# Performance work log

Hardware: AMD Instinct MI355X
Metric: run time of the kernel (lower is better)

The kernel has to match this reference:

```python
import math
import jax, jax.numpy as jnp
import numpy as np
from jax import lax

# Fixed values for the module's random shift hyperparams (in their legal ranges)
S2, S3, S5, S6 = 2, 1, -1, 1  # p_2_1_0, p_3_1_0, p_5_1_1, p_6_1_0


def setup_inputs() -> dict:
    key = jax.random.key(0)
    k1, k2, k3, k4, k5 = jax.random.split(key, 5)
    n, c, h, w = 16, 112, 48, 48
    x = jax.random.normal(k1, (n, c, h, w), dtype=jnp.float32)
    bound7 = math.sqrt(3.0 / (w * 3))
    p7_w = jax.random.uniform(k2, (3, w), minval=-bound7, maxval=bound7, dtype=jnp.float32)
    p8_w = jax.random.normal(k3, (1, c, h, 1), dtype=jnp.float32) * 0.02
    p19_w = jax.random.normal(k4, (1, c, 1, 1), dtype=jnp.float32) * 0.02
    cb = 1.0 / math.sqrt(c * 3)
    conv_w = jax.random.uniform(k5, (c, c, 1, 3), minval=-cb, maxval=cb, dtype=jnp.float32)
    return {"x": x, "p7_w": p7_w, "p8_w": p8_w, "p19_w": p19_w, "conv_w": conv_w}


def reference(x, p7_w, p8_w, p19_w, conv_w):
    n, c, h, w = x.shape
    hw = h * w
    # t_1: unfold (1,3) dilation (1,3) pad (0,3) -> width shifts of {-3,0,+3}, zero padded
    xp = jnp.pad(x, ((0, 0), (0, 0), (0, 0), (3, 3)))
    t1 = jnp.stack([xp[..., 3 * k: 3 * k + w] for k in range(3)], axis=2)  # (n,c,3,h,w)
    t2 = jnp.roll(x, S2, axis=2)
    t3 = jnp.roll(t1, S3, axis=3)
    t4 = t3.mean(axis=1)                     # (n,3,h,w)
    t5 = jnp.roll(t2, S5, axis=3)
    t6 = jnp.roll(t4, S6, axis=2)
    t7 = jnp.einsum('nkhw,kw->nh', t6, p7_w)  # einsum 'abcd,bdef->aecf' collapsed -> (n,h)
    t8 = p8_w * t5
    t9 = x + t8
    t10 = t8 - t9                             # mathematically -x, kept as written
    # p_11: Conv2d(c,c,(1,3),dilation=(1,2),padding=(0,2)), width-preserving
    t11 = lax.conv_general_dilated(
        t10, conv_w, window_strides=(1, 1), padding=((0, 0), (2, 2)),
        rhs_dilation=(1, 2), dimension_numbers=('NCHW', 'OIHW', 'NCHW'))
    # t_12: unfold (7,1) dilation (2,1) pad (6,0) on t_7 viewed (n,1,h,1)
    t7p = jnp.pad(t7, ((0, 0), (6, 6)))
    t12 = jnp.stack([t7p[:, 2 * k: 2 * k + h] for k in range(7)], axis=1)  # (n,7,h)
    t13 = jnp.maximum(t11, x)
    # t_14 = bmm(x^T, t13)/sqrt(c): (n,hw,hw)
    t14 = jnp.einsum('ncp,ncq->npq', x.reshape(n, c, hw), t13.reshape(n, c, hw)) / math.sqrt(c)
    t15 = jnp.abs(t12)
    t17 = t15.mean(axis=2)                    # (n,7)
    t18 = (t17[:, None, :] - t10.reshape(n, c * h * w // 7, 7)).reshape(n, c, h, w)
    t19 = p19_w * t18
    # t_16 = t7 - t14 (broadcast over last h*w*w of row-block view), t_20 = t7 + t16
    t14r = t14.reshape(n, h, w * h * w)
    t7b = t7[:, :, None]
    t16 = t7b - t14r
    t20 = (t7b + t16).reshape(n, hw, hw)
    t21 = jnp.einsum('ncp,npq->ncq', t19.reshape(n, c, hw), t20) / math.sqrt(hw)
    return t21.reshape(n, c, h, w)
```

## Files before the change

kernel.cpp:

```cpp
#include <hip/hip_runtime.h>

typedef __attribute__((ext_vector_type(8))) short bfrag;
typedef __attribute__((ext_vector_type(4))) float f32x4;

namespace {
constexpr int N_ = 16, C_ = 112, H_ = 48, W_ = 48, HW_ = 2304;
constexpr int NKS = 18;
constexpr int WS_T7 = 0;
constexpr int WS_A = 1024;
constexpr int WS_WPACK = 40960;
constexpr int WS_GBF = 62464;
constexpr int WS_SPART = 177152;
}

__device__ __forceinline__ float f4e(const float4& v, int e) {
  return e == 0 ? v.x : e == 1 ? v.y : e == 2 ? v.z : v.w;
}
__device__ __forceinline__ unsigned short f2bf(float f) {
  unsigned u = __float_as_uint(f);
  return (unsigned short)((u + 0x7FFFu + ((u >> 16) & 1u)) >> 16);
}
__device__ __forceinline__ float bf2f(unsigned short s) {
  return __uint_as_float(((unsigned)s) << 16);
}

__global__ __launch_bounds__(192) void ath_t7(const float* __restrict__ x,
                                              const float* __restrict__ p7,
                                              float* __restrict__ ws) {
  const int h = blockIdx.x, n = blockIdx.y;
  const int tid = threadIdx.x;
  __shared__ float q[48];
  __shared__ float wred[3];
  if (tid < 48) {
    float s = 0.f;
#pragma unroll
    for (int k = 0; k < 3; ++k) {
      int wp = tid + 3 - 3 * k;
      if (wp >= 0 && wp < 48) s += p7[k * 48 + wp];
    }
    q[tid] = s;
  }
  __syncthreads();
  const int c16 = tid / 12, qq = tid - 12 * c16;
  const float qv0 = q[4 * qq], qv1 = q[4 * qq + 1];
  const float qv2 = q[4 * qq + 2], qv3 = q[4 * qq + 3];
  float d = 0.f;
#pragma unroll
  for (int p = 0; p < 7; ++p) {
    const int c = c16 + 16 * p;
    float4 v = *(const float4*)&x[((size_t)n * C_ + c) * HW_ + h * W_ + 4 * qq];
    d += v.x * qv0 + v.y * qv1 + v.z * qv2 + v.w * qv3;
  }
#pragma unroll
  for (int off = 32; off >= 1; off >>= 1) d += __shfl_xor(d, off);
  if ((tid & 63) == 0) wred[tid >> 6] = d;
  __syncthreads();
  if (tid == 0)
    ws[WS_T7 + n * H_ + (h + 2) % 48] =
        (wred[0] + wred[1] + wred[2]) * (1.0f / 112.0f);
}

__global__ __launch_bounds__(256) void ath_gram(const float* __restrict__ x,
                                                const float* __restrict__ cw,
                                                float* __restrict__ ws) {
  const int bid = blockIdx.x;
  const int tid = threadIdx.x;
  if (bid >= 2 * NKS * N_) {
    int idx = (bid - 2 * NKS * N_) * 256 + tid;
    if (idx < 3 * 112 * 32) {
      int kx = idx / (112 * 32);
      int r = idx - kx * 112 * 32;
      int o = r >> 5;
      int i0 = (r & 31) * 4;
      unsigned short v[4];
#pragma unroll
      for (int e = 0; e < 4; ++e) {
        int i = i0 + e;
        v[e] = (i < 112) ? f2bf(cw[o * 336 + i * 3 + kx]) : (unsigned short)0;
      }
      unsigned short* wp = (unsigned short*)(ws + WS_WPACK);
      *(ushort4*)&wp[(kx * 112 + o) * 128 + i0] = make_ushort4(v[0], v[1], v[2], v[3]);
    }
    return;
  }
  const int half = bid & 1;
  const int ks = (bid >> 1) % NKS;
  const int n = bid / (2 * NKS);
  const int k0 = ks * 128;
  const int lane = tid & 63, wv = tid >> 6;
  const int lr = lane & 15, lg = lane >> 4;
  __shared__ __align__(16) unsigned short As[112][136];
  __shared__ __align__(16) unsigned short t7r[136];
  __shared__ float t7s[48];
  __shared__ float s17[8];
  if (tid < 48) t7s[tid] = ws[WS_T7 + n * H_ + tid];
  __syncthreads();
  if (tid < 7) {
    float s = 0.f;
    for (int hh = 0; hh < 48; ++hh) {
      int j = 2 * tid + hh - 6;
      if (j >= 0 && j < 48) s += fabsf(t7s[j]);
    }
    s17[tid] = s * (1.0f / 48.0f);
  }
  if (tid >= 64 && tid < 192) t7r[tid - 64] = f2bf(t7s[(k0 + tid - 64) / 48]);
  if (tid >= 192 && tid < 200) t7r[128 + (tid - 192)] = 0;
  const int ti = wv + 4 * half;
  bfrag breg[4];
  if (ti < 7) {
    const float* bp = &x[((size_t)n * C_ + 16 * ti + lr) * HW_ + k0 + 8 * lg];
#pragma unroll
    for (int kb = 0; kb < 4; ++kb) {
      float4 v0 = *(const float4*)(bp + 32 * kb);
      float4 v1 = *(const float4*)(bp + 32 * kb + 4);
      breg[kb][0] = (short)f2bf(v0.x); breg[kb][1] = (short)f2bf(v0.y);
      breg[kb][2] = (short)f2bf(v0.z); breg[kb][3] = (short)f2bf(v0.w);
      breg[kb][4] = (short)f2bf(v1.x); breg[kb][5] = (short)f2bf(v1.y);
      breg[kb][6] = (short)f2bf(v1.z); breg[kb][7] = (short)f2bf(v1.w);
    }
  }
  __syncthreads();
  const int kq = tid & 31, cg = tid >> 5;
  const int base7 = (k0 + 4 * kq) % 7;
#pragma unroll
  for (int r = 0; r < 14; ++r) {
    const int c = cg + 8 * r;
    float4 v = *(const float4*)&x[((size_t)n * C_ + c) * HW_ + k0 + 4 * kq];
    int cls0 = (base7 + c) % 7;
    unsigned short a4[4];
#pragma unroll
    for (int e = 0; e < 4; ++e) {
      int cl = cls0 + e;
      cl = (cl >= 7) ? cl - 7 : cl;
      a4[e] = f2bf(f4e(v, e) + s17[cl]);
    }
    *(ushort4*)&As[c][4 * kq] = make_ushort4(a4[0], a4[1], a4[2], a4[3]);
  }
  __syncthreads();
  if (ti == 7) {
    const bfrag zero8 = {0, 0, 0, 0, 0, 0, 0, 0};
#pragma unroll
    for (int kb = 0; kb < 4; ++kb)
      breg[kb] = (lr == 0) ? *(const bfrag*)&t7r[8 * lg + 32 * kb] : zero8;
  }
  f32x4 acc[7];
#pragma unroll
  for (int j = 0; j < 7; ++j) acc[j] = (f32x4){0.f, 0.f, 0.f, 0.f};
#pragma unroll
  for (int kb = 0; kb < 4; ++kb) {
#pragma unroll
    for (int tc = 0; tc < 7; ++tc) {
      bfrag a = *(const bfrag*)&As[16 * tc + lr][8 * lg + 32 * kb];
      acc[tc] = __builtin_amdgcn_mfma_f32_16x16x32_bf16(a, breg[kb], acc[tc], 0, 0, 0);
    }
  }
  unsigned short* sp =
      (unsigned short*)(ws + WS_SPART) + (size_t)(n * NKS + ks) * 14336;
#pragma unroll
  for (int tc = 0; tc < 7; ++tc)
#pragma unroll
    for (int e = 0; e < 4; ++e)
      sp[(16 * tc + 4 * lg + e) * 128 + 16 * ti + lr] = f2bf(acc[tc][e]);
}

__global__ __launch_bounds__(128) void ath_assemble(const float* __restrict__ p19,
                                                    float* __restrict__ ws) {
  const int bid = blockIdx.x;
  const int n = bid / 28, g = bid % 28;
  const int tid = threadIdx.x;
  const int cloc = tid >> 5, q = tid & 31;
  const int c = 4 * g + cloc;
  const int i0 = 4 * q;
  const unsigned short* spb = (const unsigned short*)(ws + WS_SPART);
  float s0 = 0.f, s1 = 0.f, s2 = 0.f, s3 = 0.f;
#pragma unroll
  for (int ks = 0; ks < NKS; ++ks) {
    ushort4 t = *(const ushort4*)&spb[(size_t)(n * NKS + ks) * 14336 + c * 128 + i0];
    s0 += bf2f(t.x); s1 += bf2f(t.y); s2 += bf2f(t.z); s3 += bf2f(t.w);
  }
  unsigned short* gb = (unsigned short*)(ws + WS_GBF);
  if (i0 < 112) {
    const float scale = 1.0f / (48.0f * sqrtf(112.0f));
    const float pc = p19[c];
    *(ushort4*)&gb[((size_t)n * C_ + c) * 128 + i0] =
        make_ushort4(f2bf(pc * s0 * scale), f2bf(pc * s1 * scale),
                     f2bf(pc * s2 * scale), f2bf(pc * s3 * scale));
  } else {
    *(ushort4*)&gb[((size_t)n * C_ + c) * 128 + i0] = make_ushort4(0, 0, 0, 0);
    if (i0 == 112) ws[WS_A + n * C_ + c] = p19[c] * s0 * (2.0f / 48.0f);
  }
}

__global__ __launch_bounds__(256) void ath_fused(const float* __restrict__ x,
                                                 const float* __restrict__ ws,
                                                 float* __restrict__ out) {
  const int h = blockIdx.x, n = blockIdx.y;
  const int tid = threadIdx.x;
  const int lane = tid & 63, wv = tid >> 6;
  const int lr = lane & 15, lg = lane >> 4;
  __shared__ __align__(16) unsigned short xT[52][136];
  __shared__ __align__(16) unsigned short buf[112][136];
  __shared__ float sA[112];
  const float* xb = x + (size_t)n * C_ * HW_ + h * W_;
  const unsigned short* wp = (const unsigned short*)(ws + WS_WPACK);
  const unsigned short* gb = (const unsigned short*)(ws + WS_GBF) + (size_t)n * C_ * 128;
  for (int idx = tid; idx < 52 * 24; idx += 256) {
    int r2 = idx / 24, cc = 112 + idx % 24;
    xT[r2][cc] = 0;
  }
  for (int idx = tid; idx < 4 * 112; idx += 256) {
    int rr = idx / 112;
    int r2 = (rr < 2) ? rr : 48 + rr;
    xT[r2][idx % 112] = 0;
  }
  if (tid < 112) sA[tid] = ws[WS_A + n * C_ + tid];
  for (int idx = tid; idx < 672; idx += 256) {
    int i2 = idx / 12, q = idx - i2 * 12;
    float4 a = *(const float4*)&xb[(size_t)(2 * i2) * HW_ + 4 * q];
    float4 b = *(const float4*)&xb[(size_t)(2 * i2 + 1) * HW_ + 4 * q];
#pragma unroll
    for (int e = 0; e < 4; ++e) {
      unsigned pk = (unsigned)f2bf(f4e(a, e)) | ((unsigned)f2bf(f4e(b, e)) << 16);
      *(unsigned*)&xT[4 * q + 2 + e][2 * i2] = pk;
    }
  }
  for (int idx = tid; idx < 1792; idx += 256) {
    int row = idx >> 4, cq = idx & 15;
    *(float4*)&buf[row][cq * 8] = *(const float4*)&wp[(size_t)row * 128 + cq * 8];
  }
  __syncthreads();

  f32x4 acc[6];
#pragma unroll
  for (int j = 0; j < 6; ++j) acc[j] = (f32x4){0.f, 0.f, 0.f, 0.f};
  for (int kx = 0; kx < 3; ++kx) {
    if (kx) {
      __syncthreads();
      for (int idx = tid; idx < 1792; idx += 256) {
        int row = idx >> 4, cq = idx & 15;
        *(float4*)&buf[row][cq * 8] =
            *(const float4*)&wp[(size_t)(kx * 112 + row) * 128 + cq * 8];
      }
      __syncthreads();
    }
#pragma unroll
    for (int j = 0; j < 6; ++j) {
      int t = wv + 4 * j;
      if (t < 21) {
        int m = t / 3, nt = t - 3 * m;
        int o0 = m * 16, w0 = nt * 16;
#pragma unroll
        for (int kb = 0; kb < 4; ++kb) {
          bfrag a = *(const bfrag*)&buf[o0 + lr][8 * lg + 32 * kb];
          bfrag b = *(const bfrag*)&xT[w0 + lr + 2 * kx][8 * lg + 32 * kb];
          acc[j] = __builtin_amdgcn_mfma_f32_16x16x32_bf16(a, b, acc[j], 0, 0, 0);
        }
      }
    }
  }
  unsigned short tv[6][4];
#pragma unroll
  for (int j = 0; j < 6; ++j) {
    int t = wv + 4 * j;
    if (t < 21) {
      int m = t / 3, nt = t - 3 * m;
      int o0 = m * 16, w0 = nt * 16;
#pragma unroll
      for (int e = 0; e < 4; ++e) {
        float xv = bf2f(xT[w0 + lr + 2][o0 + 4 * lg + e]);
        tv[j][e] = f2bf(fmaxf(-acc[j][e], xv));
      }
    }
  }
  __syncthreads();
#pragma unroll
  for (int j = 0; j < 6; ++j) {
    int t = wv + 4 * j;
    if (t < 21) {
      int m = t / 3, nt = t - 3 * m;
      int o0 = m * 16, w0 = nt * 16;
      unsigned pk0 = (unsigned)tv[j][0] | ((unsigned)tv[j][1] << 16);
      unsigned pk1 = (unsigned)tv[j][2] | ((unsigned)tv[j][3] << 16);
      *(unsigned*)&xT[w0 + lr + 2][o0 + 4 * lg] = pk0;
      *(unsigned*)&xT[w0 + lr + 2][o0 + 4 * lg + 2] = pk1;
    }
  }
  for (int idx = tid; idx < 1792; idx += 256) {
    int row = idx >> 4, cq = idx & 15;
    *(float4*)&buf[row][cq * 8] = *(const float4*)&gb[(size_t)row * 128 + cq * 8];
  }
  __syncthreads();

#pragma unroll
  for (int j = 0; j < 6; ++j) {
    int t = wv + 4 * j;
    if (t < 21) {
      int m = t / 3, nt = t - 3 * m;
      int c0 = m * 16, w0 = nt * 16;
      f32x4 acc2 = {0.f, 0.f, 0.f, 0.f};
#pragma unroll
      for (int kb = 0; kb < 4; ++kb) {
        bfrag a = *(const bfrag*)&buf[c0 + lr][8 * lg + 32 * kb];
        bfrag b = *(const bfrag*)&xT[w0 + lr + 2][8 * lg + 32 * kb];
        acc2 = __builtin_amdgcn_mfma_f32_16x16x32_bf16(a, b, acc2, 0, 0, 0);
      }
#pragma unroll
      for (int e = 0; e < 4; ++e) {
        int c = c0 + 4 * lg + e;
        out[((size_t)n * C_ + c) * HW_ + h * W_ + w0 + lr] = sA[c] - acc2[e];
      }
    }
  }
}

extern "C" void kernel_launch(void* const* d_in, const int* in_sizes, int n_in,
                              void* d_out, int out_size, void* d_ws, size_t ws_size,
                              hipStream_t stream) {
  const float* x = (const float*)d_in[0];
  const float* p7 = (const float*)d_in[1];
  const float* p19 = (const float*)d_in[3];
  const float* cw = (const float*)d_in[4];
  float* ws = (float*)d_ws;
  float* out = (float*)d_out;

  ath_t7<<<dim3(H_, N_), 192, 0, stream>>>(x, p7, ws);
  ath_gram<<<2 * NKS * N_ + 42, 256, 0, stream>>>(x, cw, ws);
  ath_assemble<<<N_ * 28, 128, 0, stream>>>(p19, ws);
  ath_fused<<<dim3(H_, N_), 256, 0, stream>>>(x, ws, out);
}
```

Baseline: 45.47 us.

## Fuse four kernels into one cooperative persistent kernel with grid syncs

Replaces the four-kernel launch sequence (t7, gram, assemble, fused conv+bmm) with a single cooperative kernel of 768 blocks that runs each stage in turn, separated by grid.sync. The assemble step (reducing the split-K partials) is folded into the conv stage so it overlaps with loading conv operands. The aim is to remove per-launch overhead and inter-kernel gaps. In exchange it needs cooperative-launch residency (3 blocks/CU, with an occupancy check and fallback to the old path) and pays for grid-wide barriers.

```diff
diff --git a/kernel.cpp b/kernel.cpp
--- a/kernel.cpp
+++ b/kernel.cpp
@@ -1,4 +1,7 @@
 #include <hip/hip_runtime.h>
+#include <hip/hip_cooperative_groups.h>
+
+namespace cg = cooperative_groups;
 
 typedef __attribute__((ext_vector_type(8))) short bfrag;
 typedef __attribute__((ext_vector_type(4))) float f32x4;
@@ -22,6 +25,296 @@
 }
 __device__ __forceinline__ float bf2f(unsigned short s) {
   return __uint_as_float(((unsigned)s) << 16);
+}
+
+__global__ __launch_bounds__(256, 3) void ath_mega(
+    const float* __restrict__ x, const float* __restrict__ p7,
+    const float* __restrict__ p19, const float* __restrict__ cw,
+    float* __restrict__ ws, float* __restrict__ out) {
+  cg::grid_group grid = cg::this_grid();
+  const int bid = blockIdx.x;
+  const int tid = threadIdx.x;
+  const int lane = tid & 63, wv = tid >> 6;
+  const int lr = lane & 15, lg = lane >> 4;
+  __shared__ __align__(16) unsigned char smem[45056];
+
+  {
+    float* q = (float*)smem;
+    float* wred = (float*)(smem + 192);
+    const int h = bid % 48, n = bid / 48;
+    if (tid < 48) {
+      float s = 0.f;
+#pragma unroll
+      for (int k = 0; k < 3; ++k) {
+        int wp = tid + 3 - 3 * k;
+        if (wp >= 0 && wp < 48) s += p7[k * 48 + wp];
+      }
+      q[tid] = s;
+    }
+    __syncthreads();
+    float d = 0.f;
+    if (tid < 192) {
+      const int c16 = tid / 12, qq = tid - 12 * c16;
+      const float qv0 = q[4 * qq], qv1 = q[4 * qq + 1];
+      const float qv2 = q[4 * qq + 2], qv3 = q[4 * qq + 3];
+#pragma unroll
+      for (int p = 0; p < 7; ++p) {
+        const int c = c16 + 16 * p;
+        float4 v = *(const float4*)&x[((size_t)n * C_ + c) * HW_ + h * W_ + 4 * qq];
+        d += v.x * qv0 + v.y * qv1 + v.z * qv2 + v.w * qv3;
+      }
+    }
+#pragma unroll
+    for (int off = 32; off >= 1; off >>= 1) d += __shfl_xor(d, off);
+    if ((tid & 63) == 0 && tid < 192) wred[tid >> 6] = d;
+    __syncthreads();
+    if (tid == 0)
+      ws[WS_T7 + (bid / 48) * H_ + ((bid % 48) + 2) % 48] =
+          (wred[0] + wred[1] + wred[2]) * (1.0f / 112.0f);
+  }
+  grid.sync();
+
+  if (bid < 2 * NKS * N_) {
+    unsigned short(*As)[136] = (unsigned short(*)[136])smem;
+    unsigned short* t7r = (unsigned short*)(smem + 30464);
+    float* t7s = (float*)(smem + 30736);
+    float* s17 = (float*)(smem + 30928);
+    const int half = bid & 1;
+    const int ks = (bid >> 1) % NKS;
+    const int n = bid / (2 * NKS);
+    const int k0 = ks * 128;
+    if (tid < 48) t7s[tid] = ws[WS_T7 + n * H_ + tid];
+    __syncthreads();
+    if (tid < 7) {
+      float s = 0.f;
+      for (int hh = 0; hh < 48; ++hh) {
+        int j = 2 * tid + hh - 6;
+        if (j >= 0 && j < 48) s += fabsf(t7s[j]);
+      }
+      s17[tid] = s * (1.0f / 48.0f);
+    }
+    if (tid >= 64 && tid < 192) t7r[tid - 64] = f2bf(t7s[(k0 + tid - 64) / 48]);
+    if (tid >= 192 && tid < 200) t7r[128 + (tid - 192)] = 0;
+    const int ti = wv + 4 * half;
+    bfrag breg[4];
+    if (ti < 7) {
+      const float* bp = &x[((size_t)n * C_ + 16 * ti + lr) * HW_ + k0 + 8 * lg];
+#pragma unroll
+      for (int kb = 0; kb < 4; ++kb) {
+        float4 v0 = *(const float4*)(bp + 32 * kb);
+        float4 v1 = *(const float4*)(bp + 32 * kb + 4);
+        breg[kb][0] = (short)f2bf(v0.x); breg[kb][1] = (short)f2bf(v0.y);
+        breg[kb][2] = (short)f2bf(v0.z); breg[kb][3] = (short)f2bf(v0.w);
+        breg[kb][4] = (short)f2bf(v1.x); breg[kb][5] = (short)f2bf(v1.y);
+        breg[kb][6] = (short)f2bf(v1.z); breg[kb][7] = (short)f2bf(v1.w);
+      }
+    }
+    __syncthreads();
+    const int kq = tid & 31, cg2 = tid >> 5;
+    const int base7 = (k0 + 4 * kq) % 7;
+#pragma unroll
+    for (int r = 0; r < 14; ++r) {
+      const int c = cg2 + 8 * r;
+      float4 v = *(const float4*)&x[((size_t)n * C_ + c) * HW_ + k0 + 4 * kq];
+      int cls0 = (base7 + c) % 7;
+      unsigned short a4[4];
+#pragma unroll
+      for (int e = 0; e < 4; ++e) {
+        int cl = cls0 + e;
+        cl = (cl >= 7) ? cl - 7 : cl;
+        a4[e] = f2bf(f4e(v, e) + s17[cl]);
+      }
+      *(ushort4*)&As[c][4 * kq] = make_ushort4(a4[0], a4[1], a4[2], a4[3]);
+    }
+    __syncthreads();
+    if (ti == 7) {
+      const bfrag zero8 = {0, 0, 0, 0, 0, 0, 0, 0};
+#pragma unroll
+      for (int kb = 0; kb < 4; ++kb)
+        breg[kb] = (lr == 0) ? *(const bfrag*)&t7r[8 * lg + 32 * kb] : zero8;
+    }
+    f32x4 acc[7];
+#pragma unroll
+    for (int j = 0; j < 7; ++j) acc[j] = (f32x4){0.f, 0.f, 0.f, 0.f};
+#pragma unroll
+    for (int kb = 0; kb < 4; ++kb) {
+#pragma unroll
+      for (int tc = 0; tc < 7; ++tc) {
+        bfrag a = *(const bfrag*)&As[16 * tc + lr][8 * lg + 32 * kb];
+        acc[tc] = __builtin_amdgcn_mfma_f32_16x16x32_bf16(a, breg[kb], acc[tc], 0, 0, 0);
+      }
+    }
+    unsigned short* sp =
+        (unsigned short*)(ws + WS_SPART) + (size_t)(n * NKS + ks) * 14336;
+#pragma unroll
+    for (int tc = 0; tc < 7; ++tc)
+#pragma unroll
+      for (int e = 0; e < 4; ++e)
+        sp[(16 * tc + 4 * lg + e) * 128 + 16 * ti + lr] = f2bf(acc[tc][e]);
+  } else if (bid < 2 * NKS * N_ + 42) {
+    int idx = (bid - 2 * NKS * N_) * 256 + tid;
+    if (idx < 3 * 112 * 32) {
+      int kx = idx / (112 * 32);
+      int r = idx - kx * 112 * 32;
+      int o = r >> 5;
+      int i0 = (r & 31) * 4;
+      unsigned short v[4];
+#pragma unroll
+      for (int e = 0; e < 4; ++e) {
+        int i = i0 + e;
+        v[e] = (i < 112) ? f2bf(cw[o * 336 + i * 3 + kx]) : (unsigned short)0;
+      }
+      unsigned short* wp = (unsigned short*)(ws + WS_WPACK);
+      *(ushort4*)&wp[(kx * 112 + o) * 128 + i0] = make_ushort4(v[0], v[1], v[2], v[3]);
+    }
+  }
+  grid.sync();
+
+  const int h = bid % 48, n = bid / 48;
+  unsigned short(*xT)[136] = (unsigned short(*)[136])smem;
+  unsigned short(*buf)[136] = (unsigned short(*)[136])(smem + 14144);
+  float* sA = (float*)(smem + 44608);
+  const float* xb = x + (size_t)n * C_ * HW_ + h * W_;
+  const unsigned short* wp = (const unsigned short*)(ws + WS_WPACK);
+  const unsigned short* gb =
+      (const unsigned short*)(ws + WS_GBF) + (size_t)n * C_ * 128;
+  {
+    for (int idx = tid; idx < 52 * 24; idx += 256) {
+      int r2 = idx / 24, cc = 112 + idx % 24;
+      xT[r2][cc] = 0;
+    }
+    for (int idx = tid; idx < 4 * 112; idx += 256) {
+      int rr = idx / 112;
+      int r2 = (rr < 2) ? rr : 48 + rr;
+      xT[r2][idx % 112] = 0;
+    }
+    for (int idx = tid; idx < 672; idx += 256) {
+      int i2 = idx / 12, q = idx - i2 * 12;
+      float4 a = *(const float4*)&xb[(size_t)(2 * i2) * HW_ + 4 * q];
+      float4 b = *(const float4*)&xb[(size_t)(2 * i2 + 1) * HW_ + 4 * q];
+#pragma unroll
+      for (int e = 0; e < 4; ++e) {
+        unsigned pk = (unsigned)f2bf(f4e(a, e)) | ((unsigned)f2bf(f4e(b, e)) << 16);
+        *(unsigned*)&xT[4 * q + 2 + e][2 * i2] = pk;
+      }
+    }
+    for (int idx = tid; idx < 1792; idx += 256) {
+      int row = idx >> 4, cq = idx & 15;
+      *(float4*)&buf[row][cq * 8] = *(const float4*)&wp[(size_t)row * 128 + cq * 8];
+    }
+    if (tid < 75) {
+      int L = bid * 75 + tid;
+      if (L < N_ * C_ * 32) {
+        int n2 = L / 3584;
+        int r = L - n2 * 3584;
+        int c2 = r >> 5;
+        int i0 = 4 * (r & 31);
+        const unsigned short* spb = (const unsigned short*)(ws + WS_SPART);
+        float s0 = 0.f, s1 = 0.f, s2 = 0.f, s3 = 0.f;
+#pragma unroll
+        for (int ks2 = 0; ks2 < NKS; ++ks2) {
+          ushort4 t =
+              *(const ushort4*)&spb[(size_t)(n2 * NKS + ks2) * 14336 + c2 * 128 + i0];
+          s0 += bf2f(t.x); s1 += bf2f(t.y); s2 += bf2f(t.z); s3 += bf2f(t.w);
+        }
+        unsigned short* gbw = (unsigned short*)(ws + WS_GBF);
+        if (i0 < 112) {
+          const float scale = 1.0f / (48.0f * sqrtf(112.0f));
+          const float pc = p19[c2];
+          *(ushort4*)&gbw[((size_t)n2 * C_ + c2) * 128 + i0] =
+              make_ushort4(f2bf(pc * s0 * scale), f2bf(pc * s1 * scale),
+                           f2bf(pc * s2 * scale), f2bf(pc * s3 * scale));
+        } else {
+          *(ushort4*)&gbw[((size_t)n2 * C_ + c2) * 128 + i0] = make_ushort4(0, 0, 0, 0);
+          if (i0 == 112) ws[WS_A + n2 * C_ + c2] = p19[c2] * s0 * (2.0f / 48.0f);
+        }
+      }
+    }
+    __syncthreads();
+    f32x4 acc[6];
+#pragma unroll
+    for (int j = 0; j < 6; ++j) acc[j] = (f32x4){0.f, 0.f, 0.f, 0.f};
+    unsigned short tv[6][4];
+    for (int kx = 0; kx < 3; ++kx) {
+      if (kx) {
+        __syncthreads();
+        for (int idx = tid; idx < 1792; idx += 256) {
+          int row = idx >> 4, cq = idx & 15;
+          *(float4*)&buf[row][cq * 8] =
+              *(const float4*)&wp[(size_t)(kx * 112 + row) * 128 + cq * 8];
+        }
+        __syncthreads();
+      }
+#pragma unroll
+      for (int j = 0; j < 6; ++j) {
+        int t = wv + 4 * j;
+        if (t < 21) {
+          int m = t / 3, nt = t - 3 * m;
+          int o0 = m * 16, w0 = nt * 16;
+#pragma unroll
+          for (int kb = 0; kb < 4; ++kb) {
+            bfrag a = *(const bfrag*)&buf[o0 + lr][8 * lg + 32 * kb];
+            bfrag b = *(const bfrag*)&xT[w0 + lr + 2 * kx][8 * lg + 32 * kb];
+            acc[j] = __builtin_amdgcn_mfma_f32_16x16x32_bf16(a, b, acc[j], 0, 0, 0);
+          }
+        }
+      }
+    }
+#pragma unroll
+    for (int j = 0; j < 6; ++j) {
+      int t = wv + 4 * j;
+      if (t < 21) {
+        int m = t / 3, nt = t - 3 * m;
+        int o0 = m * 16, w0 = nt * 16;
+#pragma unroll
+        for (int e = 0; e < 4; ++e) {
+          float xv = bf2f(xT[w0 + lr + 2][o0 + 4 * lg + e]);
+          tv[j][e] = f2bf(fmaxf(-acc[j][e], xv));
+        }
+      }
+    }
+    __syncthreads();
+#pragma unroll
+    for (int j = 0; j < 6; ++j) {
+      int t = wv + 4 * j;
+      if (t < 21) {
+        int m = t / 3, nt = t - 3 * m;
+        int o0 = m * 16, w0 = nt * 16;
+        unsigned pk0 = (unsigned)tv[j][0] | ((unsigned)tv[j][1] << 16);
+        unsigned pk1 = (unsigned)tv[j][2] | ((unsigned)tv[j][3] << 16);
+        *(unsigned*)&xT[w0 + lr + 2][o0 + 4 * lg] = pk0;
+        *(unsigned*)&xT[w0 + lr + 2][o0 + 4 * lg + 2] = pk1;
+      }
+    }
+  }
+  grid.sync();
+
+  for (int idx = tid; idx < 1792; idx += 256) {
+    int row = idx >> 4, cq = idx & 15;
+    *(float4*)&buf[row][cq * 8] = *(const float4*)&gb[(size_t)row * 128 + cq * 8];
+  }
+  if (tid < 112) sA[tid] = ws[WS_A + n * C_ + tid];
+  __syncthreads();
+#pragma unroll
+  for (int j = 0; j < 6; ++j) {
+    int t = wv + 4 * j;
+    if (t < 21) {
+      int m = t / 3, nt = t - 3 * m;
+      int c0 = m * 16, w0 = nt * 16;
+      f32x4 acc2 = {0.f, 0.f, 0.f, 0.f};
+#pragma unroll
+      for (int kb = 0; kb < 4; ++kb) {
+        bfrag a = *(const bfrag*)&buf[c0 + lr][8 * lg + 32 * kb];
+        bfrag b = *(const bfrag*)&xT[w0 + lr + 2][8 * lg + 32 * kb];
+        acc2 = __builtin_amdgcn_mfma_f32_16x16x32_bf16(a, b, acc2, 0, 0, 0);
+      }
+#pragma unroll
+      for (int e = 0; e < 4; ++e) {
+        int c = c0 + 4 * lg + e;
+        out[((size_t)n * C_ + c) * HW_ + h * W_ + w0 + lr] = sA[c] - acc2[e];
+      }
+    }
+  }
 }
 
 __global__ __launch_bounds__(192) void ath_t7(const float* __restrict__ x,
@@ -120,11 +413,11 @@
     }
   }
   __syncthreads();
-  const int kq = tid & 31, cg = tid >> 5;
+  const int kq = tid & 31, cg2 = tid >> 5;
   const int base7 = (k0 + 4 * kq) % 7;
 #pragma unroll
   for (int r = 0; r < 14; ++r) {
-    const int c = cg + 8 * r;
+    const int c = cg2 + 8 * r;
     float4 v = *(const float4*)&x[((size_t)n * C_ + c) * HW_ + k0 + 4 * kq];
     int cls0 = (base7 + c) % 7;
     unsigned short a4[4];
@@ -229,7 +522,6 @@
     *(float4*)&buf[row][cq * 8] = *(const float4*)&wp[(size_t)row * 128 + cq * 8];
   }
   __syncthreads();
-
   f32x4 acc[6];
 #pragma unroll
   for (int j = 0; j < 6; ++j) acc[j] = (f32x4){0.f, 0.f, 0.f, 0.f};
@@ -290,7 +582,6 @@
     *(float4*)&buf[row][cq * 8] = *(const float4*)&gb[(size_t)row * 128 + cq * 8];
   }
   __syncthreads();
-
 #pragma unroll
   for (int j = 0; j < 6; ++j) {
     int t = wv + 4 * j;
@@ -323,8 +614,18 @@
   float* ws = (float*)d_ws;
   float* out = (float*)d_out;
 
-  ath_t7<<<dim3(H_, N_), 192, 0, stream>>>(x, p7, ws);
-  ath_gram<<<2 * NKS * N_ + 42, 256, 0, stream>>>(x, cw, ws);
-  ath_assemble<<<N_ * 28, 128, 0, stream>>>(p19, ws);
-  ath_fused<<<dim3(H_, N_), 256, 0, stream>>>(x, ws, out);
-}
+  int maxb = 0;
+  hipError_t oe = hipOccupancyMaxActiveBlocksPerMultiprocessor(
+      &maxb, (const void*)ath_mega, 256, 0);
+  if (oe == hipSuccess && maxb >= 3) {
+    void* args[] = {(void*)&x, (void*)&p7, (void*)&p19,
+                    (void*)&cw, (void*)&ws, (void*)&out};
+    hipLaunchCooperativeKernel((void*)ath_mega, dim3(H_ * N_), dim3(256), args,
+                               0, stream);
+  } else {
+    ath_t7<<<dim3(H_, N_), 192, 0, stream>>>(x, p7, ws);
+    ath_gram<<<2 * NKS * N_ + 42, 256, 0, stream>>>(x, cw, ws);
+    ath_assemble<<<N_ * 28, 128, 0, stream>>>(p19, ws);
+    ath_fused<<<dim3(H_, N_), 256, 0, stream>>>(x, ws, out);
+  }
+}
```

Result: no change. 45.19 us (-0.6%).
